# Optimization experiments

Measured on AMD Instinct MI355X. Metric: run time of the kernel, lower is better.

Reference implementation:

```python
import jax, jax.numpy as jnp
import numpy as np

HIDDEN = 512
LATENT = 256
BATCH = 1024
SEQ_LEN = 256


def setup_inputs() -> dict:
    key = jax.random.key(0)
    ks = jax.random.split(key, 12)
    s_h = 1.0 / np.sqrt(2 * HIDDEN)
    s_c = 1.0 / np.sqrt(LATENT)
    return {
        "h": jax.random.normal(ks[0], (BATCH, HIDDEN), jnp.float32),
        "c": jax.random.normal(ks[1], (BATCH, HIDDEN), jnp.float32),
        "seq_len": SEQ_LEN,
        # init-state projections: Linear(2*hidden, latent)
        "init_h_W": jax.random.uniform(ks[2], (LATENT, 2 * HIDDEN), jnp.float32, -s_h, s_h),
        "init_h_b": jax.random.uniform(ks[3], (LATENT,), jnp.float32, -s_h, s_h),
        "init_c_W": jax.random.uniform(ks[4], (LATENT, 2 * HIDDEN), jnp.float32, -s_h, s_h),
        "init_c_b": jax.random.uniform(ks[5], (LATENT,), jnp.float32, -s_h, s_h),
        # LSTM cell: input dim = hidden, state dim = latent, gates stacked [i, f, g, o]
        "W_ih": jax.random.uniform(ks[6], (4 * LATENT, HIDDEN), jnp.float32, -s_c, s_c),
        "W_hh": jax.random.uniform(ks[7], (4 * LATENT, LATENT), jnp.float32, -s_c, s_c),
        "b_ih": jax.random.uniform(ks[8], (4 * LATENT,), jnp.float32, -s_c, s_c),
        "b_hh": jax.random.uniform(ks[9], (4 * LATENT,), jnp.float32, -s_c, s_c),
    }


def reference(h, c, seq_len, init_h_W, init_h_b, init_c_W, init_c_b, W_ih, W_hh, b_ih, b_hh):
    # init states: ELU(Linear(cat(h, c)))
    hc = jnp.concatenate([h, c], axis=1)                     # [B, 2H]
    h_t = jax.nn.elu(hc @ init_h_W.T + init_h_b)             # [B, L]
    c_t = jax.nn.elu(hc @ init_c_W.T + init_c_b)             # [B, L]

    # input to the cell is the constant encoder state h -> precompute its projection once
    x_proj = h @ W_ih.T + b_ih + b_hh                        # [B, 4L]

    def step(carry, _):
        h_t, c_t = carry
        gates = x_proj + h_t @ W_hh.T                        # [B, 4L]
        i, f, g, o = jnp.split(gates, 4, axis=1)
        c_n = jax.nn.sigmoid(f) * c_t + jax.nn.sigmoid(i) * jnp.tanh(g)
        h_n = jax.nn.sigmoid(o) * jnp.tanh(c_n)
        return (h_n, c_n), h_n

    _, ys = jax.lax.scan(step, (h_t, c_t), None, length=seq_len)  # ys: [T, B, L]
    return jnp.transpose(ys, (1, 0, 2))                      # [B, T, L]
```

## Files before the change

kernel.cpp:

```cpp
#include <hip/hip_runtime.h>
#include <stdint.h>

typedef __attribute__((ext_vector_type(4))) float f32x4;
typedef __attribute__((ext_vector_type(8))) _Float16 f16x8;

#define L_BATCH 1024
#define L_HID   512
#define L_LAT   256

static __device__ __forceinline__ unsigned short f2h(float f) {
    union { _Float16 h; unsigned short u; } v;
    v.h = (_Float16)f;
    return v.u;
}
static __device__ __forceinline__ f16x8 as_f16x8(uint4 v) {
    union { uint4 u; f16x8 s; } x; x.u = v; return x.s;
}
static __device__ __forceinline__ float sigmoid_fast(float x) {
    return __builtin_amdgcn_rcpf(1.0f + __builtin_amdgcn_exp2f(-1.4426950408889634f * x));
}
static __device__ __forceinline__ float tanh_fast(float x) {
    return 1.0f - 2.0f * __builtin_amdgcn_rcpf(1.0f + __builtin_amdgcn_exp2f(2.8853900817779268f * x));
}

__global__ void convert_strided(const float* __restrict__ src, unsigned short* __restrict__ dst,
                                int rows, int cols, int dst_stride) {
    int i = blockIdx.x * blockDim.x + threadIdx.x;
    int base = i * 4;
    if (base >= rows * cols) return;
    int r = base / cols, c = base % cols;
    float4 v = *(const float4*)(src + base);
    unsigned short* d = dst + (size_t)r * dst_stride + c;
    d[0] = f2h(v.x); d[1] = f2h(v.y); d[2] = f2h(v.z); d[3] = f2h(v.w);
}

__global__ __launch_bounds__(256) void gemm_bt(
    const unsigned short* __restrict__ A, const unsigned short* __restrict__ W,
    float* __restrict__ C, const float* __restrict__ b1, const float* __restrict__ b2,
    int K, int lda, int N, int do_elu) {
    __shared__ unsigned short As[64][40];
    __shared__ unsigned short Bs[64][40];
    int tid = threadIdx.x;
    int lane = tid & 63, wv = tid >> 6;
    int q = lane >> 4, l15 = lane & 15;
    int Mbase = blockIdx.x * 64, Nbase = blockIdx.y * 64;
    int ldrow = tid >> 2, seg = tid & 3;
    const unsigned short* Ap = A + (size_t)(Mbase + ldrow) * lda + seg * 8;
    const unsigned short* Wp = W + (size_t)(Nbase + ldrow) * K + seg * 8;
    f32x4 acc[4] = {};
    for (int k0 = 0; k0 < K; k0 += 32) {
        uint4 av = *(const uint4*)(Ap + k0);
        uint4 wvv = *(const uint4*)(Wp + k0);
        __syncthreads();
        *(uint4*)(&As[ldrow][seg * 8]) = av;
        *(uint4*)(&Bs[ldrow][seg * 8]) = wvv;
        __syncthreads();
        f16x8 af = *(const f16x8*)(&As[wv * 16 + l15][q * 8]);
#pragma unroll
        for (int nt = 0; nt < 4; nt++) {
            f16x8 bf = *(const f16x8*)(&Bs[nt * 16 + l15][q * 8]);
            acc[nt] = __builtin_amdgcn_mfma_f32_16x16x32_f16(af, bf, acc[nt], 0, 0, 0);
        }
    }
#pragma unroll
    for (int nt = 0; nt < 4; nt++) {
        int col = Nbase + nt * 16 + l15;
        float bias = b1[col] + (b2 ? b2[col] : 0.0f);
#pragma unroll
        for (int r = 0; r < 4; r++) {
            int row = Mbase + wv * 16 + q * 4 + r;
            float v = acc[nt][r] + bias;
            if (do_elu) v = v > 0.0f ? v : (__builtin_amdgcn_exp2f(1.4426950408889634f * v) - 1.0f);
            C[(size_t)row * N + col] = v;
        }
    }
}

#define HB_STRIDE 264
#define HB_HALF   (16 * HB_STRIDE)
#define WLDS_OFF  (2 * HB_HALF * 2)
#define LSTM_LDS_BYTES (WLDS_OFF + 16 * 8 * 64 * 16)

__global__ __launch_bounds__(1024) void lstm_rec(
    const unsigned short* __restrict__ Whh,
    const float* __restrict__ xp,
    const float* __restrict__ h0,
    const float* __restrict__ c0,
    const int* __restrict__ seq_len,
    float* __restrict__ out)
{
    extern __shared__ unsigned char smem[];
    unsigned short* hbuf = (unsigned short*)smem;
    unsigned char* wlds = smem + WLDS_OFF;
    int tid = threadIdx.x;
    int lane = tid & 63, wv = tid >> 6;
    int q = lane >> 4, l15 = lane & 15;
    int T = *seq_len;
    int rowbase = blockIdx.x * 16;

    const unsigned short* wbase = Whh + ((wv << 4) + l15) * 256 + q * 8;

    uint4 wreg[8];
#pragma unroll
    for (int kt = 0; kt < 2; kt++)
#pragma unroll
        for (int g = 0; g < 4; g++)
            wreg[kt * 4 + g] = *(const uint4*)(wbase + (size_t)g * 65536 + kt * 32);
#pragma unroll
    for (int kt = 2; kt < 4; kt++)
#pragma unroll
        for (int g = 0; g < 4; g++) {
            uint4 v = *(const uint4*)(wbase + (size_t)g * 65536 + kt * 32);
            *(uint4*)(wlds + ((size_t)((wv * 8) + (kt - 2) * 4 + g) * 64 + lane) * 16) = v;
        }

    float xpr[16];
#pragma unroll
    for (int g = 0; g < 4; g++)
#pragma unroll
        for (int r = 0; r < 4; r++)
            xpr[g * 4 + r] = xp[(size_t)(rowbase + q * 4 + r) * 1024 + g * 256 + wv * 16 + l15];

    float creg[4];
#pragma unroll
    for (int r = 0; r < 4; r++)
        creg[r] = c0[(size_t)(rowbase + q * 4 + r) * 256 + wv * 16 + l15];

    {
        int e = tid * 4;
        int r = e >> 8, cc = e & 255;
        float4 v = *(const float4*)(h0 + (size_t)(rowbase + r) * 256 + cc);
        unsigned short* d = hbuf + r * HB_STRIDE + cc;
        d[0] = f2h(v.x); d[1] = f2h(v.y); d[2] = f2h(v.z); d[3] = f2h(v.w);
    }
    __syncthreads();

    uint4 sbuf[4];
#pragma unroll
    for (int g = 0; g < 4; g++) sbuf[g] = *(const uint4*)(wbase + (size_t)g * 65536 + 4 * 32);

    for (int t = 0; t < T; t++) {
        unsigned short* hc = hbuf + (t & 1) * HB_HALF;
        f32x4 acc[4];
#pragma unroll
        for (int g = 0; g < 4; g++) {
            acc[g][0] = xpr[g * 4 + 0]; acc[g][1] = xpr[g * 4 + 1];
            acc[g][2] = xpr[g * 4 + 2]; acc[g][3] = xpr[g * 4 + 3];
        }
#pragma unroll
        for (int kt = 0; kt < 2; kt++) {
            f16x8 af = *(const f16x8*)(hc + l15 * HB_STRIDE + kt * 32 + q * 8);
#pragma unroll
            for (int g = 0; g < 4; g++)
                acc[g] = __builtin_amdgcn_mfma_f32_16x16x32_f16(af, as_f16x8(wreg[kt * 4 + g]), acc[g], 0, 0, 0);
        }
#pragma unroll
        for (int kt = 2; kt < 4; kt++) {
            f16x8 af = *(const f16x8*)(hc + l15 * HB_STRIDE + kt * 32 + q * 8);
#pragma unroll
            for (int g = 0; g < 4; g++) {
                f16x8 bf = *(const f16x8*)(wlds + ((size_t)((wv * 8) + (kt - 2) * 4 + g) * 64 + lane) * 16);
                acc[g] = __builtin_amdgcn_mfma_f32_16x16x32_f16(af, bf, acc[g], 0, 0, 0);
            }
        }
#pragma unroll
        for (int kt = 4; kt < 8; kt++) {
            f16x8 af = *(const f16x8*)(hc + l15 * HB_STRIDE + kt * 32 + q * 8);
            uint4 cur4[4];
#pragma unroll
            for (int g = 0; g < 4; g++) cur4[g] = sbuf[g];
            int nkt = (kt < 7) ? (kt + 1) : 4;
#pragma unroll
            for (int g = 0; g < 4; g++) sbuf[g] = *(const uint4*)(wbase + (size_t)g * 65536 + nkt * 32);
#pragma unroll
            for (int g = 0; g < 4; g++)
                acc[g] = __builtin_amdgcn_mfma_f32_16x16x32_f16(af, as_f16x8(cur4[g]), acc[g], 0, 0, 0);
        }
        unsigned short* hn = hbuf + ((t + 1) & 1) * HB_HALF;
#pragma unroll
        for (int r = 0; r < 4; r++) {
            float ig = sigmoid_fast(acc[0][r]);
            float fg = sigmoid_fast(acc[1][r]);
            float gg = tanh_fast(acc[2][r]);
            float og = sigmoid_fast(acc[3][r]);
            float cn = fg * creg[r] + ig * gg;
            creg[r] = cn;
            float hv = og * tanh_fast(cn);
            out[((size_t)(rowbase + q * 4 + r) * T + t) * 256 + wv * 16 + l15] = hv;
            hn[(q * 4 + r) * HB_STRIDE + wv * 16 + l15] = f2h(hv);
        }
        __syncthreads();
    }
}

extern "C" void kernel_launch(void* const* d_in, const int* in_sizes, int n_in,
                              void* d_out, int out_size, void* d_ws, size_t ws_size,
                              hipStream_t stream) {
    const float* h   = (const float*)d_in[0];
    const float* c   = (const float*)d_in[1];
    const int*   seqp= (const int*)d_in[2];
    const float* iWh = (const float*)d_in[3];
    const float* ibh = (const float*)d_in[4];
    const float* iWc = (const float*)d_in[5];
    const float* ibc = (const float*)d_in[6];
    const float* Wih = (const float*)d_in[7];
    const float* Whh = (const float*)d_in[8];
    const float* bih = (const float*)d_in[9];
    const float* bhh = (const float*)d_in[10];
    float* out = (float*)d_out;
    unsigned char* ws = (unsigned char*)d_ws;

    unsigned short* hc_h  = (unsigned short*)(ws + 0);
    unsigned short* iWh_h = (unsigned short*)(ws + 2097152);
    unsigned short* iWc_h = (unsigned short*)(ws + 2621440);
    unsigned short* Wih_h = (unsigned short*)(ws + 3145728);
    unsigned short* Whh_h = (unsigned short*)(ws + 4194304);
    float* h0 = (float*)(ws + 4718592);
    float* c0 = (float*)(ws + 5767168);
    float* xp = (float*)(ws + 6815744);

    hipFuncSetAttribute(reinterpret_cast<const void*>(lstm_rec),
                        hipFuncAttributeMaxDynamicSharedMemorySize, LSTM_LDS_BYTES);

    convert_strided<<<512, 256, 0, stream>>>(h,   hc_h,        1024, 512, 1024);
    convert_strided<<<512, 256, 0, stream>>>(c,   hc_h + 512,  1024, 512, 1024);
    convert_strided<<<256, 256, 0, stream>>>(iWh, iWh_h,       256, 1024, 1024);
    convert_strided<<<256, 256, 0, stream>>>(iWc, iWc_h,       256, 1024, 1024);
    convert_strided<<<512, 256, 0, stream>>>(Wih, Wih_h,       1024, 512, 512);
    convert_strided<<<256, 256, 0, stream>>>(Whh, Whh_h,       1024, 256, 256);

    gemm_bt<<<dim3(16, 4),  256, 0, stream>>>(hc_h, iWh_h, h0, ibh, nullptr, 1024, 1024, 256, 1);
    gemm_bt<<<dim3(16, 4),  256, 0, stream>>>(hc_h, iWc_h, c0, ibc, nullptr, 1024, 1024, 256, 1);
    gemm_bt<<<dim3(16, 16), 256, 0, stream>>>(hc_h, Wih_h, xp, bih, bhh,     512, 1024, 1024, 0);

    lstm_rec<<<64, 1024, LSTM_LDS_BYTES, stream>>>(Whh_h, xp, h0, c0, seqp, out);
}
```

Measured before the change: 1.389 ms.

## Merge conversion and init GEMM launches, relax LSTM barrier, interleave weight prefetch

Six fp32-to-fp16 conversion kernels become one launch, and the two init-state GEMMs become one launch with a z grid dimension. This cuts launch overhead and tail effects. In the recurrent LSTM kernel, the full __syncthreads is replaced by a barrier that waits only on LDS counters, so global output stores need not drain every step. The streamed-weight prefetch is also interleaved with the MFMAs, and launch_bounds gains an occupancy hint. The LDS-only wait relies on global stores not being read within the kernel, and the interleaved prefetch may change register pressure or latency hiding.

```diff
diff --git a/kernel.cpp b/kernel.cpp
--- a/kernel.cpp
+++ b/kernel.cpp
@@ -3,10 +3,6 @@
 
 typedef __attribute__((ext_vector_type(4))) float f32x4;
 typedef __attribute__((ext_vector_type(8))) _Float16 f16x8;
-
-#define L_BATCH 1024
-#define L_HID   512
-#define L_LAT   256
 
 static __device__ __forceinline__ unsigned short f2h(float f) {
     union { _Float16 h; unsigned short u; } v;
@@ -22,16 +18,32 @@
 static __device__ __forceinline__ float tanh_fast(float x) {
     return 1.0f - 2.0f * __builtin_amdgcn_rcpf(1.0f + __builtin_amdgcn_exp2f(2.8853900817779268f * x));
 }
-
-__global__ void convert_strided(const float* __restrict__ src, unsigned short* __restrict__ dst,
-                                int rows, int cols, int dst_stride) {
-    int i = blockIdx.x * blockDim.x + threadIdx.x;
-    int base = i * 4;
-    if (base >= rows * cols) return;
-    int r = base / cols, c = base % cols;
-    float4 v = *(const float4*)(src + base);
-    unsigned short* d = dst + (size_t)r * dst_stride + c;
-    d[0] = f2h(v.x); d[1] = f2h(v.y); d[2] = f2h(v.z); d[3] = f2h(v.w);
+static __device__ __forceinline__ void lds_barrier() {
+    __builtin_amdgcn_s_waitcnt(0xc07f);
+    __builtin_amdgcn_s_barrier();
+}
+
+__global__ __launch_bounds__(256) void convert_all(
+    const float* __restrict__ h, const float* __restrict__ c,
+    const float* __restrict__ iWh, const float* __restrict__ iWc,
+    const float* __restrict__ Wih, const float* __restrict__ Whh,
+    unsigned short* __restrict__ hc_h, unsigned short* __restrict__ iWh_h,
+    unsigned short* __restrict__ iWc_h, unsigned short* __restrict__ Wih_h,
+    unsigned short* __restrict__ Whh_h) {
+    int i = blockIdx.x * 256 + threadIdx.x;
+    const float* src; unsigned short* dst;
+    if (i < 131072) {
+        int base = i * 4, r = base >> 9, cc = base & 511;
+        src = h + base; dst = hc_h + r * 1024 + cc;
+    } else if (i < 262144) {
+        int j = i - 131072; int base = j * 4, r = base >> 9, cc = base & 511;
+        src = c + base; dst = hc_h + r * 1024 + 512 + cc;
+    } else if (i < 327680) { int j = i - 262144; src = iWh + j * 4; dst = iWh_h + j * 4; }
+    else if (i < 393216)   { int j = i - 327680; src = iWc + j * 4; dst = iWc_h + j * 4; }
+    else if (i < 524288)   { int j = i - 393216; src = Wih + j * 4; dst = Wih_h + j * 4; }
+    else                   { int j = i - 524288; src = Whh + j * 4; dst = Whh_h + j * 4; }
+    float4 v = *(const float4*)src;
+    dst[0] = f2h(v.x); dst[1] = f2h(v.y); dst[2] = f2h(v.z); dst[3] = f2h(v.w);
 }
 
 __global__ __launch_bounds__(256) void gemm_bt(
@@ -76,12 +88,58 @@
     }
 }
 
+__global__ __launch_bounds__(256) void gemm_init(
+    const unsigned short* __restrict__ A,
+    const unsigned short* __restrict__ W0, const unsigned short* __restrict__ W1,
+    float* __restrict__ C0, float* __restrict__ C1,
+    const float* __restrict__ bias0, const float* __restrict__ bias1) {
+    const unsigned short* W = blockIdx.z ? W1 : W0;
+    float* C = blockIdx.z ? C1 : C0;
+    const float* bias = blockIdx.z ? bias1 : bias0;
+    __shared__ unsigned short As[64][40];
+    __shared__ unsigned short Bs[64][40];
+    int tid = threadIdx.x;
+    int lane = tid & 63, wv = tid >> 6;
+    int q = lane >> 4, l15 = lane & 15;
+    int Mbase = blockIdx.x * 64, Nbase = blockIdx.y * 64;
+    int ldrow = tid >> 2, seg = tid & 3;
+    const unsigned short* Ap = A + (size_t)(Mbase + ldrow) * 1024 + seg * 8;
+    const unsigned short* Wp = W + (size_t)(Nbase + ldrow) * 1024 + seg * 8;
+    f32x4 acc[4] = {};
+    for (int k0 = 0; k0 < 1024; k0 += 32) {
+        uint4 av = *(const uint4*)(Ap + k0);
+        uint4 wvv = *(const uint4*)(Wp + k0);
+        __syncthreads();
+        *(uint4*)(&As[ldrow][seg * 8]) = av;
+        *(uint4*)(&Bs[ldrow][seg * 8]) = wvv;
+        __syncthreads();
+        f16x8 af = *(const f16x8*)(&As[wv * 16 + l15][q * 8]);
+#pragma unroll
+        for (int nt = 0; nt < 4; nt++) {
+            f16x8 bf = *(const f16x8*)(&Bs[nt * 16 + l15][q * 8]);
+            acc[nt] = __builtin_amdgcn_mfma_f32_16x16x32_f16(af, bf, acc[nt], 0, 0, 0);
+        }
+    }
+#pragma unroll
+    for (int nt = 0; nt < 4; nt++) {
+        int col = Nbase + nt * 16 + l15;
+        float b = bias[col];
+#pragma unroll
+        for (int r = 0; r < 4; r++) {
+            int row = Mbase + wv * 16 + q * 4 + r;
+            float v = acc[nt][r] + b;
+            v = v > 0.0f ? v : (__builtin_amdgcn_exp2f(1.4426950408889634f * v) - 1.0f);
+            C[(size_t)row * 256 + col] = v;
+        }
+    }
+}
+
 #define HB_STRIDE 264
 #define HB_HALF   (16 * HB_STRIDE)
 #define WLDS_OFF  (2 * HB_HALF * 2)
 #define LSTM_LDS_BYTES (WLDS_OFF + 16 * 8 * 64 * 16)
 
-__global__ __launch_bounds__(1024) void lstm_rec(
+__global__ __launch_bounds__(1024, 4) void lstm_rec(
     const unsigned short* __restrict__ Whh,
     const float* __restrict__ xp,
     const float* __restrict__ h0,
@@ -166,15 +224,12 @@
 #pragma unroll
         for (int kt = 4; kt < 8; kt++) {
             f16x8 af = *(const f16x8*)(hc + l15 * HB_STRIDE + kt * 32 + q * 8);
-            uint4 cur4[4];
-#pragma unroll
-            for (int g = 0; g < 4; g++) cur4[g] = sbuf[g];
             int nkt = (kt < 7) ? (kt + 1) : 4;
 #pragma unroll
-            for (int g = 0; g < 4; g++) sbuf[g] = *(const uint4*)(wbase + (size_t)g * 65536 + nkt * 32);
-#pragma unroll
-            for (int g = 0; g < 4; g++)
-                acc[g] = __builtin_amdgcn_mfma_f32_16x16x32_f16(af, as_f16x8(cur4[g]), acc[g], 0, 0, 0);
+            for (int g = 0; g < 4; g++) {
+                acc[g] = __builtin_amdgcn_mfma_f32_16x16x32_f16(af, as_f16x8(sbuf[g]), acc[g], 0, 0, 0);
+                sbuf[g] = *(const uint4*)(wbase + (size_t)g * 65536 + nkt * 32);
+            }
         }
         unsigned short* hn = hbuf + ((t + 1) & 1) * HB_HALF;
 #pragma unroll
@@ -189,7 +244,7 @@
             out[((size_t)(rowbase + q * 4 + r) * T + t) * 256 + wv * 16 + l15] = hv;
             hn[(q * 4 + r) * HB_STRIDE + wv * 16 + l15] = f2h(hv);
         }
-        __syncthreads();
+        lds_barrier();
     }
 }
 
@@ -222,16 +277,11 @@
     hipFuncSetAttribute(reinterpret_cast<const void*>(lstm_rec),
                         hipFuncAttributeMaxDynamicSharedMemorySize, LSTM_LDS_BYTES);
 
-    convert_strided<<<512, 256, 0, stream>>>(h,   hc_h,        1024, 512, 1024);
-    convert_strided<<<512, 256, 0, stream>>>(c,   hc_h + 512,  1024, 512, 1024);
-    convert_strided<<<256, 256, 0, stream>>>(iWh, iWh_h,       256, 1024, 1024);
-    convert_strided<<<256, 256, 0, stream>>>(iWc, iWc_h,       256, 1024, 1024);
-    convert_strided<<<512, 256, 0, stream>>>(Wih, Wih_h,       1024, 512, 512);
-    convert_strided<<<256, 256, 0, stream>>>(Whh, Whh_h,       1024, 256, 256);
-
-    gemm_bt<<<dim3(16, 4),  256, 0, stream>>>(hc_h, iWh_h, h0, ibh, nullptr, 1024, 1024, 256, 1);
-    gemm_bt<<<dim3(16, 4),  256, 0, stream>>>(hc_h, iWc_h, c0, ibc, nullptr, 1024, 1024, 256, 1);
-    gemm_bt<<<dim3(16, 16), 256, 0, stream>>>(hc_h, Wih_h, xp, bih, bhh,     512, 1024, 1024, 0);
+    convert_all<<<2304, 256, 0, stream>>>(h, c, iWh, iWc, Wih, Whh,
+                                          hc_h, iWh_h, iWc_h, Wih_h, Whh_h);
+
+    gemm_init<<<dim3(16, 4, 2), 256, 0, stream>>>(hc_h, iWh_h, iWc_h, h0, c0, ibh, ibc);
+    gemm_bt<<<dim3(16, 16), 256, 0, stream>>>(hc_h, Wih_h, xp, bih, bhh, 512, 1024, 1024, 0);
 
     lstm_rec<<<64, 1024, LSTM_LDS_BYTES, stream>>>(Whh_h, xp, h0, c0, seqp, out);
 }
```

After: 1.355 ms. -2.5%, faster.
